# Optimization experiments

Hardware: AMD Instinct MI355X
Metric: run time of the kernel (lower is better)

Reference implementation:

```python
import jax, jax.numpy as jnp
import numpy as np

NUM_EXPERTS = 64
TOP_K = 8
NORM_TOPK_PROB = True


def setup_inputs() -> dict:
    key = jax.random.key(0)
    k1, k2 = jax.random.split(key)
    hidden_states = jax.random.normal(k1, (8192, 4096), dtype=jnp.float32)
    gate_w = jax.random.normal(k2, (NUM_EXPERTS, 4096), dtype=jnp.float32) * (1.0 / np.sqrt(4096))
    return {"hidden_states": hidden_states, "gate_w": gate_w}


def reference(hidden_states, gate_w):
    # router_logits: (T, E) = hidden @ gate_w.T
    router_logits = jnp.einsum('th,eh->te', hidden_states, gate_w)
    # softmax in float32 (matches F.softmax(..., dtype=torch.float32))
    router_probs = jax.nn.softmax(router_logits.astype(jnp.float32), axis=-1)
    # top-k selection (descending, like torch.topk)
    expert_weights, expert_indices = jax.lax.top_k(router_probs, TOP_K)
    if NORM_TOPK_PROB:
        expert_weights = expert_weights / jnp.sum(expert_weights, axis=-1, keepdims=True)
    expert_weights = expert_weights.astype(hidden_states.dtype)
    # load-balancing loss: N_e * sum_i f_i * p_i
    num_tokens = router_probs.shape[0]
    one_hot = jax.nn.one_hot(expert_indices, NUM_EXPERTS, dtype=jnp.float32)  # (T, K, E)
    tokens_per_expert = one_hot.sum(axis=(0, 1))                              # (E,)
    f = tokens_per_expert / (num_tokens * TOP_K)
    p = router_probs.mean(axis=0)
    aux_loss = NUM_EXPERTS * jnp.sum(f * p)
    return (expert_weights, expert_indices, aux_loss)
```

## Files before the change

kernel.cpp:

```cpp
#include <hip/hip_runtime.h>
#include <math.h>

#define HDIM 4096
#define NEXP 64
#define NTOK 8192
#define KSPLIT 4
#define KSLICE (HDIM / KSPLIT)
#define NCHUNK (KSLICE / 32)
#define NKC (HDIM / 32)
#define AUXF 1024
#define TPW 2
#define BT_TERM (NKC * 4 * 64 * 8)
#define BT_KC (4 * 64 * 8)

typedef short short8 __attribute__((ext_vector_type(8)));
typedef float f32x4 __attribute__((ext_vector_type(4)));

union i4s8 { int4 i; short8 s; };

__device__ __forceinline__ void split2x3(float x0, float x1, int& h, int& md, int& lo) {
  unsigned u0 = __float_as_uint(x0), u1 = __float_as_uint(x1);
  unsigned h0 = u0 & 0xFFFF0000u, h1 = u1 & 0xFFFF0000u;
  float r0 = x0 - __uint_as_float(h0);
  float r1 = x1 - __uint_as_float(h1);
  unsigned m0 = __float_as_uint(r0) & 0xFFFF0000u;
  unsigned m1 = __float_as_uint(r1) & 0xFFFF0000u;
  float s0 = r0 - __uint_as_float(m0);
  float s1 = r1 - __uint_as_float(m1);
  h  = (int)((h0 >> 16) | h1);
  md = (int)((m0 >> 16) | m1);
  lo = (int)((__float_as_uint(s0) >> 16) | (__float_as_uint(s1) & 0xFFFF0000u));
}

__device__ __forceinline__ void split8v(const f32x4& p0, const f32x4& p1,
                                        short8& h8, short8& m8, short8& l8) {
  i4s8 h, m, l;
  split2x3(p0.x, p0.y, h.i.x, m.i.x, l.i.x);
  split2x3(p0.z, p0.w, h.i.y, m.i.y, l.i.y);
  split2x3(p1.x, p1.y, h.i.z, m.i.z, l.i.z);
  split2x3(p1.z, p1.w, h.i.w, m.i.w, l.i.w);
  h8 = h.s; m8 = m.s; l8 = l.s;
}

__global__ __launch_bounds__(256) void prep_k(const float* __restrict__ W,
                                              short* __restrict__ Bs,
                                              float* __restrict__ auxbuf) {
  if (blockIdx.x == 128) {
#pragma unroll
    for (int j = 0; j < 4; ++j) auxbuf[j * 256 + threadIdx.x] = 0.f;
    return;
  }
  const int g = blockIdx.x * 256 + threadIdx.x;
  const int n = g >> 9;
  const int k8 = g & 511;
  const f32x4 p0 = *(const f32x4*)&W[(size_t)n * HDIM + k8 * 8];
  const f32x4 p1 = *(const f32x4*)&W[(size_t)n * HDIM + k8 * 8 + 4];
  short8 h8, m8, l8;
  split8v(p0, p1, h8, m8, l8);
  const int kc = k8 >> 2, quad = k8 & 3;
  const size_t o = (((size_t)kc * 4 + quad) * 64 + n) * 8;
  *(short8*)&Bs[o] = h8;
  *(short8*)&Bs[o + BT_TERM] = m8;
  *(short8*)&Bs[o + 2 * BT_TERM] = l8;
}

__device__ __forceinline__ f32x4 ntload4(const float* p) {
  return __builtin_nontemporal_load((const f32x4*)p);
}

__device__ __forceinline__ void loadB(const short* bc, short8* b) {
#pragma unroll
  for (int nt = 0; nt < 4; ++nt) {
    b[nt]     = *(const short8*)(bc + nt * 128);
    b[4 + nt] = *(const short8*)(bc + nt * 128 + BT_TERM);
    b[8 + nt] = *(const short8*)(bc + nt * 128 + 2 * BT_TERM);
  }
}

__global__ __launch_bounds__(256, 3) void gemm_k(const float* __restrict__ A,
                                                 const short* __restrict__ Bs,
                                                 float* __restrict__ Lp,
                                                 int atomic_mode) {
  const int tid = threadIdx.x;
  const int wave = tid >> 6, lane = tid & 63;
  const int l15 = lane & 15, quad = lane >> 4;
  const int m_base = blockIdx.x * 64 + wave * 16;
  const int kb = blockIdx.y;
  float* Lout = Lp + (atomic_mode ? (size_t)0 : (size_t)kb * NTOK * NEXP);

  const float* a0 = A + (size_t)(m_base + l15) * HDIM + kb * KSLICE + quad * 8;
  const short* bbase = Bs + ((size_t)(kb * NCHUNK) * 4 + quad) * 512 + l15 * 8;

  f32x4 acc[4];
#pragma unroll
  for (int nt = 0; nt < 4; ++nt) acc[nt] = (f32x4){0.f, 0.f, 0.f, 0.f};

  short8 B[2][12];
  f32x4 ra[2][2];
  short8 fa[3];

  loadB(bbase, B[0]);
  ra[0][0] = ntload4(a0);
  ra[0][1] = ntload4(a0 + 4);
  ra[1][0] = ntload4(a0 + 32);
  ra[1][1] = ntload4(a0 + 36);

#pragma unroll 2
  for (int i = 0; i < NCHUNK; ++i) {
    const int cur = i & 1;
    const int ip1 = (i + 1 < NCHUNK) ? i + 1 : i;
    loadB(bbase + (size_t)ip1 * BT_KC, B[cur ^ 1]);
    split8v(ra[cur][0], ra[cur][1], fa[0], fa[1], fa[2]);
    if (i + 2 < NCHUNK) {
      ra[cur][0] = ntload4(a0 + (i + 2) * 32);
      ra[cur][1] = ntload4(a0 + (i + 2) * 32 + 4);
    }
#pragma unroll
    for (int nt = 0; nt < 4; ++nt) {
      f32x4 c = acc[nt];
      c = __builtin_amdgcn_mfma_f32_16x16x32_bf16(fa[0], B[cur][nt], c, 0, 0, 0);
      c = __builtin_amdgcn_mfma_f32_16x16x32_bf16(fa[0], B[cur][4 + nt], c, 0, 0, 0);
      c = __builtin_amdgcn_mfma_f32_16x16x32_bf16(fa[1], B[cur][nt], c, 0, 0, 0);
      c = __builtin_amdgcn_mfma_f32_16x16x32_bf16(fa[0], B[cur][8 + nt], c, 0, 0, 0);
      c = __builtin_amdgcn_mfma_f32_16x16x32_bf16(fa[2], B[cur][nt], c, 0, 0, 0);
      c = __builtin_amdgcn_mfma_f32_16x16x32_bf16(fa[1], B[cur][4 + nt], c, 0, 0, 0);
      acc[nt] = c;
    }
  }

#pragma unroll
  for (int nt = 0; nt < 4; ++nt)
#pragma unroll
    for (int r = 0; r < 4; ++r) {
      const int m = m_base + quad * 4 + r;
      const int n = nt * 16 + l15;
      if (atomic_mode) atomicAdd(&Lout[(size_t)m * NEXP + n], acc[nt][r]);
      else Lout[(size_t)m * NEXP + n] = acc[nt][r];
    }
}

__global__ __launch_bounds__(256) void topk_k(const float* __restrict__ Lp, int nsl,
                                              float* __restrict__ out,
                                              float* __restrict__ auxbuf) {
  __shared__ float sl[4][64];
  __shared__ float s_aux[128];
  const int tid = threadIdx.x;
  const int wave = tid >> 6, lane = tid & 63;
  if (tid < 128) s_aux[tid] = 0.f;
  __syncthreads();

  for (int it = 0; it < TPW; ++it) {
    const int t = (blockIdx.x * 4 + wave) * TPW + it;
    float x = 0.f;
    for (int s = 0; s < nsl; ++s)
      x += Lp[(size_t)s * (NTOK * NEXP) + (size_t)t * NEXP + lane];
    sl[wave][lane] = x;

    float mx = x;
#pragma unroll
    for (int off = 32; off >= 1; off >>= 1)
      mx = fmaxf(mx, __shfl_xor(mx, off, 64));
    const float e = __expf(x - mx);
    float ssum = e;
#pragma unroll
    for (int off = 32; off >= 1; off >>= 1) ssum += __shfl_xor(ssum, off, 64);
    const float prob = e / ssum;

    __syncthreads();

    int cnt = 0;
#pragma unroll
    for (int c = 0; c < 4; ++c) {
      const float4 v0 = *(const float4*)&sl[wave][c * 16 + 0];
      const float4 v1 = *(const float4*)&sl[wave][c * 16 + 4];
      const float4 v2 = *(const float4*)&sl[wave][c * 16 + 8];
      const float4 v3 = *(const float4*)&sl[wave][c * 16 + 12];
      const float xv[16] = {v0.x, v0.y, v0.z, v0.w, v1.x, v1.y, v1.z, v1.w,
                            v2.x, v2.y, v2.z, v2.w, v3.x, v3.y, v3.z, v3.w};
#pragma unroll
      for (int j = 0; j < 16; ++j) {
        const int jj = c * 16 + j;
        cnt += (xv[j] > x) || (xv[j] == x && jj < lane);
      }
    }

    float tp = (cnt < 8) ? prob : 0.f;
    float tsum = tp;
#pragma unroll
    for (int off = 32; off >= 1; off >>= 1) tsum += __shfl_xor(tsum, off, 64);

    const int dst = cnt << 2;
    const float pv = __uint_as_float(
        (unsigned)__builtin_amdgcn_ds_permute(dst, (int)__float_as_uint(prob)));
    const int pi = __builtin_amdgcn_ds_permute(dst, lane);
    if (lane < 8) {
      out[(size_t)t * 8 + lane] = pv / tsum;
      out[(size_t)NTOK * 8 + (size_t)t * 8 + lane] = (float)pi;
    }
    atomicAdd(&s_aux[lane], prob);
    if (cnt < 8) atomicAdd(&s_aux[64 + lane], 1.f);
  }
  __syncthreads();
  if (tid < 128) atomicAdd(&auxbuf[(blockIdx.x & 7) * 128 + tid], s_aux[tid]);
}

__global__ void aux_k(const float* __restrict__ auxbuf, float* __restrict__ out) {
  const int e = threadIdx.x;
  float p = 0.f, f = 0.f;
#pragma unroll
  for (int c = 0; c < 8; ++c) {
    p += auxbuf[c * 128 + e];
    f += auxbuf[c * 128 + 64 + e];
  }
  p *= (1.f / (float)NTOK);
  f *= (1.f / ((float)NTOK * 8.f));
  float v = f * p;
#pragma unroll
  for (int off = 32; off >= 1; off >>= 1) v += __shfl_xor(v, off, 64);
  if (e == 0) out[2 * NTOK * 8] = 64.f * v;
}

extern "C" void kernel_launch(void* const* d_in, const int* in_sizes, int n_in,
                              void* d_out, int out_size, void* d_ws, size_t ws_size,
                              hipStream_t stream) {
  const float* hidden = (const float*)d_in[0];
  const float* gate = (const float*)d_in[1];
  float* out = (float*)d_out;
  float* ws = (float*)d_ws;
  float* auxbuf = ws;

  const size_t full_need =
      (size_t)AUXF * 4 + (size_t)KSPLIT * NTOK * NEXP * 4 + (size_t)3 * BT_TERM * 2 + 4096;
  const int atomic_mode = (ws_size < full_need) ? 1 : 0;
  const int nsl = atomic_mode ? 1 : KSPLIT;
  float* slices = ws + AUXF;
  short* Bs = (short*)(ws + AUXF + (size_t)nsl * NTOK * NEXP);

  if (atomic_mode)
    (void)hipMemsetAsync(slices, 0, (size_t)NTOK * NEXP * 4, stream);

  prep_k<<<129, 256, 0, stream>>>(gate, Bs, auxbuf);
  gemm_k<<<dim3(128, KSPLIT), 256, 0, stream>>>(hidden, Bs, slices, atomic_mode);
  topk_k<<<NTOK / (4 * TPW), 256, 0, stream>>>(slices, nsl, out, auxbuf);
  aux_k<<<1, 64, 0, stream>>>(auxbuf, out);
}
```

Measured before the change: 240.5 us.

## Stage split gate weights through LDS with direct global-to-LDS loads, double KSPLIT

Each wave used to load every B fragment (hi/mid/lo bf16 parts) from global memory into registers, so the four waves in a block fetched the same data redundantly. Now the block cooperatively copies each K-chunk of B into double-buffered shared memory with global_load_lds, and every wave reads its fragments from LDS, with a barrier per chunk. Freeing those registers lets occupancy rise to 4 blocks per SIMD unit. KSPLIT goes from 4 to 8, which doubles the partial-logit slices the top-k kernel must sum and the workspace they need, in exchange for more parallel blocks.

New measurement: 221.4 us. -7.9%, faster.

```diff
diff --git a/kernel.cpp b/kernel.cpp
--- a/kernel.cpp
+++ b/kernel.cpp
@@ -4,7 +4,7 @@
 #define HDIM 4096
 #define NEXP 64
 #define NTOK 8192
-#define KSPLIT 4
+#define KSPLIT 8
 #define KSLICE (HDIM / KSPLIT)
 #define NCHUNK (KSLICE / 32)
 #define NKC (HDIM / 32)
@@ -42,6 +42,16 @@
   h8 = h.s; m8 = m.s; l8 = l.s;
 }
 
+__device__ __forceinline__ f32x4 ntload4(const float* p) {
+  return __builtin_nontemporal_load((const f32x4*)p);
+}
+
+__device__ __forceinline__ void cp16(const void* g, void* l) {
+  __builtin_amdgcn_global_load_lds(
+      (const __attribute__((address_space(1))) unsigned int*)g,
+      (__attribute__((address_space(3))) unsigned int*)l, 16, 0, 0);
+}
+
 __global__ __launch_bounds__(256) void prep_k(const float* __restrict__ W,
                                               short* __restrict__ Bs,
                                               float* __restrict__ auxbuf) {
@@ -64,23 +74,11 @@
   *(short8*)&Bs[o + 2 * BT_TERM] = l8;
 }
 
-__device__ __forceinline__ f32x4 ntload4(const float* p) {
-  return __builtin_nontemporal_load((const f32x4*)p);
-}
-
-__device__ __forceinline__ void loadB(const short* bc, short8* b) {
-#pragma unroll
-  for (int nt = 0; nt < 4; ++nt) {
-    b[nt]     = *(const short8*)(bc + nt * 128);
-    b[4 + nt] = *(const short8*)(bc + nt * 128 + BT_TERM);
-    b[8 + nt] = *(const short8*)(bc + nt * 128 + 2 * BT_TERM);
-  }
-}
-
-__global__ __launch_bounds__(256, 3) void gemm_k(const float* __restrict__ A,
+__global__ __launch_bounds__(256, 4) void gemm_k(const float* __restrict__ A,
                                                  const short* __restrict__ Bs,
                                                  float* __restrict__ Lp,
                                                  int atomic_mode) {
+  __shared__ __align__(16) short Blds[2][6144];
   const int tid = threadIdx.x;
   const int wave = tid >> 6, lane = tid & 63;
   const int l15 = lane & 15, quad = lane >> 4;
@@ -89,43 +87,53 @@
   float* Lout = Lp + (atomic_mode ? (size_t)0 : (size_t)kb * NTOK * NEXP);
 
   const float* a0 = A + (size_t)(m_base + l15) * HDIM + kb * KSLICE + quad * 8;
-  const short* bbase = Bs + ((size_t)(kb * NCHUNK) * 4 + quad) * 512 + l15 * 8;
+  const short* bsrc = Bs + (size_t)(kb * NCHUNK) * BT_KC + (wave * 64 + lane) * 8;
 
   f32x4 acc[4];
 #pragma unroll
   for (int nt = 0; nt < 4; ++nt) acc[nt] = (f32x4){0.f, 0.f, 0.f, 0.f};
 
-  short8 B[2][12];
   f32x4 ra[2][2];
   short8 fa[3];
 
-  loadB(bbase, B[0]);
-  ra[0][0] = ntload4(a0);
-  ra[0][1] = ntload4(a0 + 4);
-  ra[1][0] = ntload4(a0 + 32);
-  ra[1][1] = ntload4(a0 + 36);
+  auto stageB = [&](int buf, int i) {
+#pragma unroll
+    for (int j = 0; j < 3; ++j)
+      cp16(bsrc + (size_t)j * BT_TERM + (size_t)i * BT_KC,
+           &Blds[buf][(j * 4 + wave) * 512]);
+  };
+  auto loadA = [&](int buf, int i) {
+    ra[buf][0] = ntload4(a0 + i * 32);
+    ra[buf][1] = ntload4(a0 + i * 32 + 4);
+  };
+
+  stageB(0, 0);
+  loadA(0, 0);
+  loadA(1, 1);
+  __syncthreads();
 
 #pragma unroll 2
   for (int i = 0; i < NCHUNK; ++i) {
     const int cur = i & 1;
-    const int ip1 = (i + 1 < NCHUNK) ? i + 1 : i;
-    loadB(bbase + (size_t)ip1 * BT_KC, B[cur ^ 1]);
+    if (i + 1 < NCHUNK) stageB(cur ^ 1, i + 1);
     split8v(ra[cur][0], ra[cur][1], fa[0], fa[1], fa[2]);
-    if (i + 2 < NCHUNK) {
-      ra[cur][0] = ntload4(a0 + (i + 2) * 32);
-      ra[cur][1] = ntload4(a0 + (i + 2) * 32 + 4);
-    }
+    if (i + 2 < NCHUNK) loadA(cur, i + 2);
+    const int fo = quad * 512 + l15 * 8;
 #pragma unroll
     for (int nt = 0; nt < 4; ++nt) {
+      const short8 bh = *(const short8*)&Blds[cur][fo + nt * 128];
+      const short8 bm = *(const short8*)&Blds[cur][2048 + fo + nt * 128];
+      const short8 bl = *(const short8*)&Blds[cur][4096 + fo + nt * 128];
       f32x4 c = acc[nt];
-      c = __builtin_amdgcn_mfma_f32_16x16x32_bf16(fa[0], B[cur][nt], c, 0, 0, 0);
-      c = __builtin_amdgcn_mfma_f32_16x16x32_bf16(fa[0], B[cur][4 + nt], c, 0, 0, 0);
-      c = __builtin_amdgcn_mfma_f32_16x16x32_bf16(fa[1], B[cur][nt], c, 0, 0, 0);
-      c = __builtin_amdgcn_mfma_f32_16x16x32_bf16(fa[0], B[cur][8 + nt], c, 0, 0, 0);
-      c = __builtin_amdgcn_mfma_f32_16x16x32_bf16(fa[2], B[cur][nt], c, 0, 0, 0);
-      c = __builtin_amdgcn_mfma_f32_16x16x32_bf16(fa[1], B[cur][4 + nt], c, 0, 0, 0);
+      c = __builtin_amdgcn_mfma_f32_16x16x32_bf16(fa[0], bh, c, 0, 0, 0);
+      c = __builtin_amdgcn_mfma_f32_16x16x32_bf16(fa[0], bm, c, 0, 0, 0);
+      c = __builtin_amdgcn_mfma_f32_16x16x32_bf16(fa[1], bh, c, 0, 0, 0);
+      c = __builtin_amdgcn_mfma_f32_16x16x32_bf16(fa[0], bl, c, 0, 0, 0);
+      c = __builtin_amdgcn_mfma_f32_16x16x32_bf16(fa[2], bh, c, 0, 0, 0);
+      c = __builtin_amdgcn_mfma_f32_16x16x32_bf16(fa[1], bm, c, 0, 0, 0);
       acc[nt] = c;
     }
+    __syncthreads();
   }
 
 #pragma unroll
```
